# Performance work log

Hardware: AMD Instinct MI355X
Metric: run time of the kernel (lower is better)

The kernel has to match this reference:

```python
import jax, jax.numpy as jnp
import numpy as np

TAU = 2.0
ALPHA = 4.0  # spikingjelly surrogate.Sigmoid default
NUM_HEADS = 8


def lif(x, v_th):
    # Multi-step LIF over leading time axis T. v_reset=0, hard reset, tau=2.
    # Forward: Heaviside spike; backward: sigmoid surrogate via straight-through.
    def step(v, xt):
        v = v + (xt - v) / TAU
        hard = (v >= v_th).astype(xt.dtype)
        soft = jax.nn.sigmoid(ALPHA * (v - v_th))
        spike = soft + jax.lax.stop_gradient(hard - soft)
        v = v * (1.0 - jax.lax.stop_gradient(hard))  # detach_reset hard reset to 0
        return v, spike
    _, out = jax.lax.scan(step, jnp.zeros_like(x[0]), x)
    return out


def conv_bn_lif(x, w, scale, bias, v_th=1.0):
    # 1x1 conv (no bias) + folded eval-mode BatchNorm + LIF.
    # x: [T,B,C,H,W], w: [Cout,Cin], scale/bias: [Cout]
    y = jnp.einsum('tbchw,dc->tbdhw', x, w)
    y = y * scale[:, None, None] + bias[:, None, None]
    return lif(y, v_th)


def setup_inputs() -> dict:
    key = jax.random.key(0)
    ks = jax.random.split(key, 14)
    T, B, C, H, W = 4, 32, 384, 14, 14
    x = jax.random.normal(ks[0], (T, B, C, H, W), dtype=jnp.float32)
    def conv_params(k):
        k1, k2, k3 = jax.random.split(k, 3)
        w = jax.random.normal(k1, (C, C), dtype=jnp.float32) * (1.0 / np.sqrt(C))
        scale = jax.random.uniform(k2, (C,), dtype=jnp.float32, minval=0.5, maxval=1.5)
        bias = jax.random.normal(k3, (C,), dtype=jnp.float32) * 0.1
        return w, scale, bias
    wq, sq, bq = conv_params(ks[1])
    wk, sk, bk = conv_params(ks[2])
    wv, sv, bv = conv_params(ks[3])
    wp, sp, bp = conv_params(ks[4])
    return {"x": x, "wq": wq, "sq": sq, "bq": bq, "wk": wk, "sk": sk, "bk": bk,
            "wv": wv, "sv": sv, "bv": bv, "wp": wp, "sp": sp, "bp": bp}


def reference(x, wq, sq, bq, wk, sk, bk, wv, sv, bv, wp, sp, bp):
    T, B, C, H, W = x.shape
    h = NUM_HEADS
    d = C // h
    N = H * W
    # QKV: conv+BN+LIF -> binary spikes [T,B,C,H,W]
    qs = conv_bn_lif(x, wq, sq, bq)
    ks_ = conv_bn_lif(x, wk, sk, bk)
    vs = conv_bn_lif(x, wv, sv, bv)
    # [T,B,C,H,W] -> [T,B,h,d,N] -> [T,B,h,N,d]
    def to_heads(t):
        return t.reshape(T, B, h, d, N).transpose(0, 1, 2, 4, 3)
    q, k, v = to_heads(qs), to_heads(ks_), to_heads(vs)
    attn = jnp.einsum('tbhnd,tbhmd->tbhnm', q, k)
    out = jnp.einsum('tbhnm,tbhmd->tbhnd', attn, v) * 0.125
    out = lif(out, 0.5)  # attn_lif v_threshold=0.5
    # [T,B,h,N,d] -> [T,B,h,d,N] -> [T,B,C,H,W]
    out = out.transpose(0, 1, 2, 4, 3).reshape(T, B, C, H, W)
    out = conv_bn_lif(out, wp, sp, bp)
    return out
```

## Files before the change

### kernel.cpp

```cpp
#include <hip/hip_runtime.h>


#define T_ 4
#define B_ 32
#define C_ 384
#define N_ 196
#define NH_ 8
#define D_ 48
#define TB_ (T_ * B_)
#define CN_ ((size_t)C_ * N_)
#define BCN4_ (B_ * C_ * (N_ / 4))
#define TBCN_ ((size_t)T_ * B_ * C_ * N_)

__global__ __launch_bounds__(256, 2) void gemm_f32(
    const float* __restrict__ X, const float* __restrict__ W0,
    const float* __restrict__ W1, const float* __restrict__ W2,
    float* __restrict__ P)
{
  const int g = blockIdx.z;
  const float* __restrict__ W = (g == 0) ? W0 : (g == 1) ? W1 : W2;
  const int co0 = blockIdx.y * 128;
  const int j0 = blockIdx.x * 128;
  __shared__ float As[16][128];
  __shared__ float Bs[16][128];
  const int tid = threadIdx.x;
  const int tx = tid & 15, ty = tid >> 4;

  const int bcol = (tid & 31) * 4;
  const int bk = tid >> 5;
  const int bj = j0 + bcol;
  const int btb = bj / N_;
  const float* xb = X + (size_t)btb * CN_ + (bj - btb * N_);
  const int arow = tid >> 1;
  const int ac8 = (tid & 1) * 8;

  float acc[8][8] = {};
  for (int c0 = 0; c0 < C_; c0 += 16) {
    const float* wrow = W + (size_t)(co0 + arow) * C_ + c0 + ac8;
    const float4 a0 = *(const float4*)wrow;
    const float4 a1 = *(const float4*)(wrow + 4);
    As[ac8 + 0][arow] = a0.x; As[ac8 + 1][arow] = a0.y;
    As[ac8 + 2][arow] = a0.z; As[ac8 + 3][arow] = a0.w;
    As[ac8 + 4][arow] = a1.x; As[ac8 + 5][arow] = a1.y;
    As[ac8 + 6][arow] = a1.z; As[ac8 + 7][arow] = a1.w;
    *(float4*)&Bs[bk][bcol]     = *(const float4*)(xb + (size_t)(c0 + bk) * N_);
    *(float4*)&Bs[bk + 8][bcol] = *(const float4*)(xb + (size_t)(c0 + bk + 8) * N_);
    __syncthreads();
#pragma unroll
    for (int k = 0; k < 16; ++k) {
      float a[8], b[8];
      *(float4*)&a[0] = *(const float4*)&As[k][ty * 4];
      *(float4*)&a[4] = *(const float4*)&As[k][64 + ty * 4];
      *(float4*)&b[0] = *(const float4*)&Bs[k][tx * 4];
      *(float4*)&b[4] = *(const float4*)&Bs[k][64 + tx * 4];
#pragma unroll
      for (int i = 0; i < 8; ++i)
#pragma unroll
        for (int j = 0; j < 8; ++j)
          acc[i][j] = fmaf(a[i], b[j], acc[i][j]);
    }
    __syncthreads();
  }
#pragma unroll
  for (int cg = 0; cg < 2; ++cg) {
    const int jj = j0 + cg * 64 + tx * 4;
    const int tb = jj / N_;
    float* pb = P + (size_t)(g * TB_ + tb) * CN_ + (jj - tb * N_);
#pragma unroll
    for (int rg = 0; rg < 2; ++rg) {
#pragma unroll
      for (int i = 0; i < 4; ++i) {
        const int r = rg * 4 + i;
        const int co = co0 + rg * 64 + ty * 4 + i;
        *(float4*)&pb[(size_t)co * N_] = make_float4(
            acc[r][cg * 4 + 0], acc[r][cg * 4 + 1],
            acc[r][cg * 4 + 2], acc[r][cg * 4 + 3]);
      }
    }
  }
}

__global__ __launch_bounds__(256) void lif4(
    const float* __restrict__ In, float* __restrict__ Out,
    const float* __restrict__ s0, const float* __restrict__ b0,
    const float* __restrict__ s1, const float* __restrict__ b1,
    const float* __restrict__ s2, const float* __restrict__ b2,
    float vth, int ng)
{
  const long u = (long)blockIdx.x * 256 + threadIdx.x;
  if (u >= (long)ng * BCN4_) return;
  const int g = (int)(u / BCN4_);
  const long r = u % BCN4_;
  const int c = (int)((r / (N_ / 4)) % C_);
  const float* sp = (g == 0) ? s0 : (g == 1) ? s1 : s2;
  const float* bp = (g == 0) ? b0 : (g == 1) ? b1 : b2;
  const bool has_bn = (sp != nullptr);
  const float sc = has_bn ? sp[c] : 1.0f;
  const float bi = has_bn ? bp[c] : 0.0f;
  const float4* In4 = (const float4*)In;
  float4* Out4 = (float4*)Out;
  float v[4] = {0.f, 0.f, 0.f, 0.f};
#pragma unroll
  for (int t = 0; t < T_; ++t) {
    const long idx = (long)(g * T_ + t) * BCN4_ + r;
    const float4 y4 = In4[idx];
    float y[4] = {y4.x, y4.y, y4.z, y4.w};
    float o[4];
#pragma unroll
    for (int e = 0; e < 4; ++e) {
      const float yb = has_bn ? __fadd_rn(__fmul_rn(y[e], sc), bi) : y[e];
      v[e] = __fadd_rn(v[e], __fmul_rn(__fsub_rn(yb, v[e]), 0.5f));
      const bool fire = (v[e] >= vth);
      o[e] = fire ? 1.0f : 0.0f;
      v[e] = fire ? 0.0f : v[e];
    }
    Out4[idx] = make_float4(o[0], o[1], o[2], o[3]);
  }
}

__global__ __launch_bounds__(256) void attn196(
    const float* __restrict__ Q, const float* __restrict__ K,
    const float* __restrict__ V, float* __restrict__ O)
{
  const int h = blockIdx.x, tb = blockIdx.y;
  __shared__ unsigned long long qb[N_], kb[N_];
  __shared__ float vsh[N_][D_];
  const int tid = threadIdx.x;
  const size_t base = ((size_t)tb * C_ + h * D_) * N_;
  if (tid < N_) {
    unsigned long long qm = 0ull, km = 0ull;
    for (int dd = 0; dd < D_; ++dd) {
      if (Q[base + (size_t)dd * N_ + tid] > 0.5f) qm |= 1ull << dd;
      if (K[base + (size_t)dd * N_ + tid] > 0.5f) km |= 1ull << dd;
    }
    qb[tid] = qm; kb[tid] = km;
  }
  for (int u = tid; u < N_ * D_; u += 256) {
    const int dd = u / N_, m = u % N_;
    vsh[m][dd] = V[base + (size_t)dd * N_ + m];
  }
  __syncthreads();
  if (tid < N_) {
    const unsigned long long qm = qb[tid];
    float out[D_];
#pragma unroll
    for (int i = 0; i < D_; ++i) out[i] = 0.f;
    for (int m = 0; m < N_; ++m) {
      const float s = (float)__popcll(qm & kb[m]);
      const float4* vp = (const float4*)&vsh[m][0];
#pragma unroll
      for (int i = 0; i < D_ / 4; ++i) {
        const float4 vv = vp[i];
        out[4 * i + 0] = fmaf(s, vv.x, out[4 * i + 0]);
        out[4 * i + 1] = fmaf(s, vv.y, out[4 * i + 1]);
        out[4 * i + 2] = fmaf(s, vv.z, out[4 * i + 2]);
        out[4 * i + 3] = fmaf(s, vv.w, out[4 * i + 3]);
      }
    }
    for (int dd = 0; dd < D_; ++dd)
      O[base + (size_t)dd * N_ + tid] = out[dd] * 0.125f;
  }
}

extern "C" void kernel_launch(void* const* d_in, const int* in_sizes, int n_in,
                              void* d_out, int out_size, void* d_ws, size_t ws_size,
                              hipStream_t stream) {
  const float* x  = (const float*)d_in[0];
  const float* wq = (const float*)d_in[1];
  const float* sq = (const float*)d_in[2];
  const float* bq = (const float*)d_in[3];
  const float* wk = (const float*)d_in[4];
  const float* sk = (const float*)d_in[5];
  const float* bk = (const float*)d_in[6];
  const float* wv = (const float*)d_in[7];
  const float* sv = (const float*)d_in[8];
  const float* bv = (const float*)d_in[9];
  const float* wp = (const float*)d_in[10];
  const float* sp = (const float*)d_in[11];
  const float* bp = (const float*)d_in[12];
  float* out = (float*)d_out;

  float* P = (float*)d_ws;
  float* O = P + 3 * TBCN_;
  float* P2 = P;

  gemm_f32<<<dim3(196, 3, 3), 256, 0, stream>>>(x, wq, wk, wv, P);
  lif4<<<dim3(3 * BCN4_ / 256), 256, 0, stream>>>(P, P, sq, bq, sk, bk, sv, bv, 1.0f, 3);
  attn196<<<dim3(NH_, TB_), 256, 0, stream>>>(P, P + TBCN_, P + 2 * TBCN_, O);
  lif4<<<dim3(BCN4_ / 256), 256, 0, stream>>>(O, O, nullptr, nullptr, nullptr,
                                              nullptr, nullptr, nullptr, 0.5f, 1);
  gemm_f32<<<dim3(196, 3, 1), 256, 0, stream>>>(O, wp, wp, wp, P2);
  lif4<<<dim3(BCN4_ / 256), 256, 0, stream>>>(P2, out, sp, bp, nullptr, nullptr,
                                              nullptr, nullptr, 1.0f, 1);
}
```

Before: 587.9 us.

## Fuse QKV LIF, reassociated spike attention, and attn LIF into one kernel

```diff
diff --git a/kernel.cpp b/kernel.cpp
--- a/kernel.cpp
+++ b/kernel.cpp
@@ -11,6 +11,7 @@
 #define CN_ ((size_t)C_ * N_)
 #define BCN4_ (B_ * C_ * (N_ / 4))
 #define TBCN_ ((size_t)T_ * B_ * C_ * N_)
+typedef unsigned long long u64;
 
 __global__ __launch_bounds__(256, 2) void gemm_f32(
     const float* __restrict__ X, const float* __restrict__ W0,
@@ -82,27 +83,21 @@
 
 __global__ __launch_bounds__(256) void lif4(
     const float* __restrict__ In, float* __restrict__ Out,
-    const float* __restrict__ s0, const float* __restrict__ b0,
-    const float* __restrict__ s1, const float* __restrict__ b1,
-    const float* __restrict__ s2, const float* __restrict__ b2,
-    float vth, int ng)
+    const float* __restrict__ s0, const float* __restrict__ b0, float vth)
 {
   const long u = (long)blockIdx.x * 256 + threadIdx.x;
-  if (u >= (long)ng * BCN4_) return;
-  const int g = (int)(u / BCN4_);
-  const long r = u % BCN4_;
+  if (u >= BCN4_) return;
+  const long r = u;
   const int c = (int)((r / (N_ / 4)) % C_);
-  const float* sp = (g == 0) ? s0 : (g == 1) ? s1 : s2;
-  const float* bp = (g == 0) ? b0 : (g == 1) ? b1 : b2;
-  const bool has_bn = (sp != nullptr);
-  const float sc = has_bn ? sp[c] : 1.0f;
-  const float bi = has_bn ? bp[c] : 0.0f;
+  const bool has_bn = (s0 != nullptr);
+  const float sc = has_bn ? s0[c] : 1.0f;
+  const float bi = has_bn ? b0[c] : 0.0f;
   const float4* In4 = (const float4*)In;
   float4* Out4 = (float4*)Out;
   float v[4] = {0.f, 0.f, 0.f, 0.f};
 #pragma unroll
   for (int t = 0; t < T_; ++t) {
-    const long idx = (long)(g * T_ + t) * BCN4_ + r;
+    const long idx = (long)t * BCN4_ + r;
     const float4 y4 = In4[idx];
     float y[4] = {y4.x, y4.y, y4.z, y4.w};
     float o[4];
@@ -118,47 +113,95 @@
   }
 }
 
-__global__ __launch_bounds__(256) void attn196(
-    const float* __restrict__ Q, const float* __restrict__ K,
-    const float* __restrict__ V, float* __restrict__ O)
+__global__ __launch_bounds__(1024) void fused_attn(
+    const float* __restrict__ P, float* __restrict__ O,
+    const float* __restrict__ sq, const float* __restrict__ bq,
+    const float* __restrict__ sk, const float* __restrict__ bk,
+    const float* __restrict__ sv, const float* __restrict__ bv)
 {
-  const int h = blockIdx.x, tb = blockIdx.y;
-  __shared__ unsigned long long qb[N_], kb[N_];
-  __shared__ float vsh[N_][D_];
+  const int h = blockIdx.x;
+  const int b = blockIdx.y;
+  __shared__ u64 msk[3][T_][D_][4];
+  __shared__ float G[D_][52];
   const int tid = threadIdx.x;
-  const size_t base = ((size_t)tb * C_ + h * D_) * N_;
-  if (tid < N_) {
-    unsigned long long qm = 0ull, km = 0ull;
-    for (int dd = 0; dd < D_; ++dd) {
-      if (Q[base + (size_t)dd * N_ + tid] > 0.5f) qm |= 1ull << dd;
-      if (K[base + (size_t)dd * N_ + tid] > 0.5f) km |= 1ull << dd;
-    }
-    qb[tid] = qm; kb[tid] = km;
-  }
-  for (int u = tid; u < N_ * D_; u += 256) {
-    const int dd = u / N_, m = u % N_;
-    vsh[m][dd] = V[base + (size_t)dd * N_ + m];
+  const int wave = tid >> 6, lane = tid & 63;
+
+  for (int task = wave; task < 3 * D_ * 4; task += 16) {
+    const int g = task / (D_ * 4);
+    const int rem = task - g * (D_ * 4);
+    const int j = rem >> 2, w = rem & 3;
+    const int m = w * 64 + lane;
+    const bool act = (m < N_);
+    const int mc = act ? m : (N_ - 1);
+    const int c = h * D_ + j;
+    const float sc = (g == 0 ? sq : g == 1 ? sk : sv)[c];
+    const float bi = (g == 0 ? bq : g == 1 ? bk : bv)[c];
+    const float* base = P + (size_t)g * TB_ * CN_ + (size_t)b * CN_
+                          + (size_t)c * N_ + mc;
+    float v = 0.f;
+#pragma unroll
+    for (int t = 0; t < T_; ++t) {
+      const float y = base[(size_t)t * B_ * CN_];
+      const float yb = __fadd_rn(__fmul_rn(y, sc), bi);
+      v = __fadd_rn(v, __fmul_rn(__fsub_rn(yb, v), 0.5f));
+      const bool fire = (v >= 1.0f);
+      if (fire) v = 0.f;
+      const u64 bl = __ballot(fire && act);
+      if (lane == 0) msk[g][t][j][w] = bl;
+    }
   }
   __syncthreads();
-  if (tid < N_) {
-    const unsigned long long qm = qb[tid];
-    float out[D_];
-#pragma unroll
-    for (int i = 0; i < D_; ++i) out[i] = 0.f;
-    for (int m = 0; m < N_; ++m) {
-      const float s = (float)__popcll(qm & kb[m]);
-      const float4* vp = (const float4*)&vsh[m][0];
-#pragma unroll
-      for (int i = 0; i < D_ / 4; ++i) {
-        const float4 vv = vp[i];
-        out[4 * i + 0] = fmaf(s, vv.x, out[4 * i + 0]);
-        out[4 * i + 1] = fmaf(s, vv.y, out[4 * i + 1]);
-        out[4 * i + 2] = fmaf(s, vv.z, out[4 * i + 2]);
-        out[4 * i + 3] = fmaf(s, vv.w, out[4 * i + 3]);
+
+  const int u = tid;
+  const bool ow = (u < 4 * N_);
+  const int dq = ow ? (u / N_) : 0;
+  const int n = ow ? (u - dq * N_) : 0;
+  const int d0 = dq * 12;
+  const int nw = n >> 6, nb = n & 63;
+  float vmem[12];
+#pragma unroll
+  for (int i = 0; i < 12; ++i) vmem[i] = 0.f;
+
+  for (int t = 0; t < T_; ++t) {
+    for (int e = tid; e < D_ * D_; e += 1024) {
+      const int j = e / D_, d = e - j * D_;
+      const u64* kj = msk[1][t][j];
+      const u64* vd = msk[2][t][d];
+      const int s = __popcll(kj[0] & vd[0]) + __popcll(kj[1] & vd[1]) +
+                    __popcll(kj[2] & vd[2]) + __popcll(kj[3] & vd[3]);
+      G[j][d] = (float)s;
+    }
+    __syncthreads();
+    if (ow) {
+      float out[12];
+#pragma unroll
+      for (int i = 0; i < 12; ++i) out[i] = 0.f;
+#pragma unroll 4
+      for (int j = 0; j < D_; ++j) {
+        const u64 qw = msk[0][t][j][nw];
+        const float qf = (float)((qw >> nb) & 1ull);
+        const float* Gj = &G[j][d0];
+        const float4 g0 = *(const float4*)&Gj[0];
+        const float4 g1 = *(const float4*)&Gj[4];
+        const float4 g2 = *(const float4*)&Gj[8];
+        out[0] = fmaf(qf, g0.x, out[0]);  out[1] = fmaf(qf, g0.y, out[1]);
+        out[2] = fmaf(qf, g0.z, out[2]);  out[3] = fmaf(qf, g0.w, out[3]);
+        out[4] = fmaf(qf, g1.x, out[4]);  out[5] = fmaf(qf, g1.y, out[5]);
+        out[6] = fmaf(qf, g1.z, out[6]);  out[7] = fmaf(qf, g1.w, out[7]);
+        out[8] = fmaf(qf, g2.x, out[8]);  out[9] = fmaf(qf, g2.y, out[9]);
+        out[10] = fmaf(qf, g2.z, out[10]); out[11] = fmaf(qf, g2.w, out[11]);
       }
-    }
-    for (int dd = 0; dd < D_; ++dd)
-      O[base + (size_t)dd * N_ + tid] = out[dd] * 0.125f;
+      float* ob = O + ((size_t)(t * B_ + b) * C_ + h * D_ + d0) * N_ + n;
+#pragma unroll
+      for (int i = 0; i < 12; ++i) {
+        const float y = out[i] * 0.125f;
+        vmem[i] = __fadd_rn(vmem[i], __fmul_rn(__fsub_rn(y, vmem[i]), 0.5f));
+        const bool fire = (vmem[i] >= 0.5f);
+        ob[(size_t)i * N_] = fire ? 1.0f : 0.0f;
+        if (fire) vmem[i] = 0.f;
+      }
+    }
+    __syncthreads();
   }
 }
 
@@ -185,11 +228,7 @@
   float* P2 = P;
 
   gemm_f32<<<dim3(196, 3, 3), 256, 0, stream>>>(x, wq, wk, wv, P);
-  lif4<<<dim3(3 * BCN4_ / 256), 256, 0, stream>>>(P, P, sq, bq, sk, bk, sv, bv, 1.0f, 3);
-  attn196<<<dim3(NH_, TB_), 256, 0, stream>>>(P, P + TBCN_, P + 2 * TBCN_, O);
-  lif4<<<dim3(BCN4_ / 256), 256, 0, stream>>>(O, O, nullptr, nullptr, nullptr,
-                                              nullptr, nullptr, nullptr, 0.5f, 1);
+  fused_attn<<<dim3(NH_, B_), 1024, 0, stream>>>(P, O, sq, bq, sk, bk, sv, bv);
   gemm_f32<<<dim3(196, 3, 1), 256, 0, stream>>>(O, wp, wp, wp, P2);
-  lif4<<<dim3(BCN4_ / 256), 256, 0, stream>>>(P2, out, sp, bp, nullptr, nullptr,
-                                              nullptr, nullptr, 1.0f, 1);
-}
+  lif4<<<dim3((BCN4_ + 255) / 256), 256, 0, stream>>>(P2, out, sp, bp, 1.0f);
+}
```

After: 540.1 us. 8.1% less time.
